# Performance work log

Hardware: AMD Instinct MI355X
Metric: run time of the kernel (lower is better)

The kernel has to match this reference:

```python
import jax, jax.numpy as jnp
import numpy as np

HEIGHT = 8  # init kwarg: output crop height
B, J, C, HIMG, WIMG = 8, 64, 32, 256, 256


def _make_boxes():
    rng = np.random.default_rng(0)
    left = rng.uniform(0.0, 40.0, (B, J))
    bw = rng.uniform(16.0, 200.0, (B, J))
    top = rng.uniform(0.0, 200.0, (B, J))
    bh = rng.uniform(8.0, 32.0, (B, J))
    theta = rng.uniform(-0.5, 0.5, (B, J))  # unused by the original forward
    return np.stack([left, top, left + bw, top + bh, theta], axis=-1).astype(np.float32)


def _box_widths(boxes_np):
    # torch: width = int(aspect * height), truncation (values are positive)
    bw = boxes_np[..., 2] - boxes_np[..., 0]
    bh = boxes_np[..., 3] - boxes_np[..., 1]
    return ((bw / bh) * HEIGHT).astype(np.int32)  # [B, J]


def setup_inputs() -> dict:
    key = jax.random.key(0)
    image = jax.random.normal(key, (B, C, HIMG, WIMG), dtype=jnp.float32)
    boxes = jnp.asarray(_make_boxes())
    return {"image": image, "boxes": boxes}


def reference(image, boxes):
    # Per-box widths are integer (shape-determining) constants, taken from concrete box data.
    boxes_np = np.asarray(jax.device_get(boxes))
    widths_np = _box_widths(boxes_np)          # [B, J] ints >= 2
    max_w = int(widths_np.max())
    widths = jnp.asarray(widths_np)

    dt = boxes.dtype
    base_w = boxes[..., 2] - boxes[..., 0]      # [B, J]
    base_h = boxes[..., 3] - boxes[..., 1]
    each_w = base_w / (widths.astype(dt) - 1)   # [B, J]
    each_h = base_h / (HEIGHT - 1)

    # Sampling grids: xx [B,J,Wm], yy [B,J,Hh]
    xx = jnp.arange(max_w, dtype=dt)[None, None, :] * each_w[..., None] + boxes[..., 0:1]
    yy = jnp.arange(HEIGHT, dtype=dt)[None, None, :] * each_h[..., None] + boxes[..., 1:2]

    def interp_one_image(img, x, y):
        # img [C,Hi,Wi], x [J,Wm], y [J,Hh] -> [C,J,Hh,Wm]
        x0 = jnp.clip(jnp.floor(x).astype(jnp.int32), 0, WIMG - 1)
        x1 = jnp.clip(jnp.floor(x).astype(jnp.int32) + 1, 0, WIMG - 1)
        y0 = jnp.clip(jnp.floor(y).astype(jnp.int32), 0, HIMG - 1)
        y1 = jnp.clip(jnp.floor(y).astype(jnp.int32) + 1, 0, HIMG - 1)
        # gathers: [C, J, Hh, Wm]
        ia = img[:, y0[:, :, None], x0[:, None, :]]
        ib = img[:, y1[:, :, None], x0[:, None, :]]
        ic = img[:, y0[:, :, None], x1[:, None, :]]
        idd = img[:, y1[:, :, None], x1[:, None, :]]
        x0f, x1f = x0.astype(dt), x1.astype(dt)
        y0f, y1f = y0.astype(dt), y1.astype(dt)
        wa = (x1f - x)[:, None, :] * (y1f - y)[:, :, None]  # [J,Hh,Wm]
        wb = (x1f - x)[:, None, :] * (y - y0f)[:, :, None]
        wc = (x - x0f)[:, None, :] * (y1f - y)[:, :, None]
        wd = (x - x0f)[:, None, :] * (y - y0f)[:, :, None]
        return ia * wa[None] + ib * wb[None] + ic * wc[None] + idd * wd[None]

    res = jax.vmap(interp_one_image)(image, xx, yy)      # [B,C,J,Hh,Wm]
    res = jnp.transpose(res, (0, 2, 1, 3, 4))            # [B,J,C,Hh,Wm]

    mask = (jnp.arange(max_w)[None, None, :] < widths[..., None]).astype(jnp.uint8)  # [B,J,Wm]
    res = res * mask[:, :, None, None, :].astype(res.dtype)  # zero-pad beyond each box width
    return res, mask
```

## Files before the change

kernel.cpp:

```cpp
#include <hip/hip_runtime.h>

#define HIMG 256
#define WIMG 256
#define CCH  32
#define JBOX 64
#define BIMG 8
#define HGT  8
#define CPB  4
#define NCG  (CCH / CPB)
#define NXCD 8
#define LROW 256

typedef __attribute__((address_space(3))) float lds_f;
typedef const __attribute__((address_space(1))) float glb_f;

#define WAITV2() do { asm volatile("s_waitcnt vmcnt(2)" ::: "memory"); \
                      __builtin_amdgcn_sched_barrier(0); } while (0)

__global__ __launch_bounds__(256, 8) void roi_kernel(
    const float* __restrict__ img,
    const float* __restrict__ boxes,
    float* __restrict__ res,
    float* __restrict__ mask,
    int max_w)
{
    __shared__ float sbuf[2][CPB][2][LROW];

    const int d    = blockIdx.x;
    const int slot = d & (NXCD - 1);
    const int seq  = d >> 3;
    const int bj   = slot * ((BIMG * JBOX) / NXCD) + (seq >> 3);
    const int cg   = seq & 7;
    const int b    = bj >> 6;
    const int tid  = threadIdx.x;

    const float left = boxes[bj * 5 + 0];
    const float top  = boxes[bj * 5 + 1];
    const float bw   = boxes[bj * 5 + 2] - left;
    const float bh   = boxes[bj * 5 + 3] - top;

    const int   width  = (int)(bw / bh * 8.0f);
    const float each_w = bw / ((float)width - 1.0f);
    const float each_h = bh / 7.0f;

    const int xs  = max((int)floorf(left), 0);
    const int xs4 = xs & ~3;

    const int  i    = tid;
    const bool have = (i < max_w);
    const bool in_w = (i < width);
    const float x  = __fadd_rn(__fmul_rn((float)i, each_w), left);
    const int   xf = (int)floorf(x);
    const int   x0 = min(max(xf, 0), WIMG - 1);
    const float wx1 = (float)(x0 + 1) - x;
    const float wx0 = x - (float)x0;
    const int   lx0 = min(max(x0 - xs4, 0), 206);

    if (cg == 0 && have) {
        mask[(size_t)bj * max_w + i] = in_w ? 1.0f : 0.0f;
    }

    const int wv   = tid >> 6;
    const int lane = tid & 63;
    const float* chbase =
        img + (size_t)(b * CCH + cg * CPB + wv) * (HIMG * WIMG);
    const int offc = min(xs4 + 4 * lane, WIMG - 4);

    auto issue_batch = [&](int h, int bf) {
        const float yh  = __fadd_rn(__fmul_rn((float)h, each_h), top);
        const int   yfl = (int)floorf(yh);
        const int   ya  = min(max(yfl,     0), HIMG - 1);
        const int   yb  = min(max(yfl + 1, 0), HIMG - 1);
        const float* s0 = chbase + (size_t)ya * WIMG + offc;
        const float* s1 = chbase + (size_t)yb * WIMG + offc;
        __builtin_amdgcn_global_load_lds((glb_f*)s0, (lds_f*)&sbuf[bf][wv][0][0], 16, 0, 0);
        __builtin_amdgcn_global_load_lds((glb_f*)s1, (lds_f*)&sbuf[bf][wv][1][0], 16, 0, 0);
    };

    issue_batch(0, 0);
    issue_batch(1, 1);
    __builtin_amdgcn_sched_barrier(0);

    float* resp0 = res + ((size_t)(bj * CCH + cg * CPB) * HGT) * (size_t)max_w + i;
    const size_t c_stride = (size_t)HGT * max_w;

    #pragma unroll
    for (int h = 0; h < HGT; ++h) {
        const int bf = h & 1;

        WAITV2();
        __builtin_amdgcn_s_barrier();
        __builtin_amdgcn_sched_barrier(0);

        if (have) {
            const float yh  = __fadd_rn(__fmul_rn((float)h, each_h), top);
            const int   yfl = (int)floorf(yh);
            const int   ya  = min(max(yfl,     0), HIMG - 1);
            const int   yb  = min(max(yfl + 1, 0), HIMG - 1);
            const float wy1 = (float)yb - yh;
            const float wy0 = yh - (float)ya;
            const float wa  = wx1 * wy1;
            const float wb_ = wx1 * wy0;
            const float wc_ = wx0 * wy1;
            const float wd_ = wx0 * wy0;
            float* resp = resp0 + (size_t)h * max_w;
            #pragma unroll
            for (int c = 0; c < CPB; ++c) {
                const float v00 = sbuf[bf][c][0][lx0];
                const float v01 = sbuf[bf][c][0][lx0 + 1];
                const float v10 = sbuf[bf][c][1][lx0];
                const float v11 = sbuf[bf][c][1][lx0 + 1];
                const float val = v00 * wa + v10 * wb_ + v01 * wc_ + v11 * wd_;
                resp[(size_t)c * c_stride] = in_w ? val : 0.0f;
            }
        }

        __builtin_amdgcn_sched_barrier(0);
        __builtin_amdgcn_s_barrier();
        __builtin_amdgcn_sched_barrier(0);

        if (h + 2 < HGT) {
            issue_batch(h + 2, bf);
            __builtin_amdgcn_sched_barrier(0);
        }
    }
}

extern "C" void kernel_launch(void* const* d_in, const int* in_sizes, int n_in,
                              void* d_out, int out_size, void* d_ws, size_t ws_size,
                              hipStream_t stream) {
    const float* img   = (const float*)d_in[0];
    const float* boxes = (const float*)d_in[1];
    float* out = (float*)d_out;

    const int per_w = BIMG * JBOX * CCH * HGT + BIMG * JBOX;
    const int max_w = out_size / per_w;

    float* res  = out;
    float* mask = out + (size_t)BIMG * JBOX * CCH * HGT * max_w;

    const int blocks = BIMG * JBOX * NCG;
    roi_kernel<<<blocks, 256, 0, stream>>>(img, boxes, res, mask, max_w);
}
```

Before: 153.3 us.

## Stage each box's full row band per channel in LDS with one block per channel

Each block now handles a single (box, channel) pair instead of four channels. It first loads every image row the box's eight sample heights can touch, full width, into LDS with direct global-to-LDS loads behind one barrier. The eight output rows are then interpolated from that staged band. This removes the per-height double-buffered pipeline and its repeated barriers, and launches more, smaller blocks (192 threads). In exchange it loads more image data per channel and assumes max_w fits in 192 threads and the row span fits in 34 rows.

Result: slower. 170.2 us (+11.0%).

```diff
diff --git a/kernel.cpp b/kernel.cpp
--- a/kernel.cpp
+++ b/kernel.cpp
@@ -6,33 +6,27 @@
 #define JBOX 64
 #define BIMG 8
 #define HGT  8
-#define CPB  4
-#define NCG  (CCH / CPB)
-#define NXCD 8
-#define LROW 256
+#define MAXR 34
 
 typedef __attribute__((address_space(3))) float lds_f;
 typedef const __attribute__((address_space(1))) float glb_f;
 
-#define WAITV2() do { asm volatile("s_waitcnt vmcnt(2)" ::: "memory"); \
-                      __builtin_amdgcn_sched_barrier(0); } while (0)
-
-__global__ __launch_bounds__(256, 8) void roi_kernel(
+__global__ __launch_bounds__(192, 3) void roi_kernel(
     const float* __restrict__ img,
     const float* __restrict__ boxes,
     float* __restrict__ res,
     float* __restrict__ mask,
     int max_w)
 {
-    __shared__ float sbuf[2][CPB][2][LROW];
+    __shared__ float srows[MAXR][WIMG];
 
-    const int d    = blockIdx.x;
-    const int slot = d & (NXCD - 1);
-    const int seq  = d >> 3;
-    const int bj   = slot * ((BIMG * JBOX) / NXCD) + (seq >> 3);
-    const int cg   = seq & 7;
-    const int b    = bj >> 6;
-    const int tid  = threadIdx.x;
+    const int g   = blockIdx.x;
+    const int b   = g & 7;
+    const int idx = g >> 3;
+    const int c   = idx >> 6;
+    const int j   = idx & 63;
+    const int bj  = b * JBOX + j;
+    const int tid = threadIdx.x;
 
     const float left = boxes[bj * 5 + 0];
     const float top  = boxes[bj * 5 + 1];
@@ -43,86 +37,59 @@
     const float each_w = bw / ((float)width - 1.0f);
     const float each_h = bh / 7.0f;
 
-    const int xs  = max((int)floorf(left), 0);
-    const int xs4 = xs & ~3;
+    const int   ylo = min(max((int)floorf(top), 0), HIMG - 1);
+    const float y7  = __fadd_rn(__fmul_rn(7.0f, each_h), top);
+    const int   yhi = min(max((int)floorf(y7) + 1, 0), HIMG - 1);
+    const int   nr  = min(yhi - ylo + 1, MAXR);
 
-    const int  i    = tid;
-    const bool have = (i < max_w);
+    const int wv   = tid >> 6;
+    const int lane = tid & 63;
+    const float* chbase = img + (size_t)(b * CCH + c) * (HIMG * WIMG);
+    for (int r = wv; r < nr; r += 3) {
+        const float* src = chbase + (size_t)(ylo + r) * WIMG + 4 * lane;
+        __builtin_amdgcn_global_load_lds((glb_f*)src, (lds_f*)&srows[r][0], 16, 0, 0);
+    }
+    __syncthreads();
+
+    const int  i = tid;
+    if (i >= max_w) return;
     const bool in_w = (i < width);
+
+    if (c == 0) {
+        mask[(size_t)bj * max_w + i] = in_w ? 1.0f : 0.0f;
+    }
+
     const float x  = __fadd_rn(__fmul_rn((float)i, each_w), left);
     const int   xf = (int)floorf(x);
     const int   x0 = min(max(xf, 0), WIMG - 1);
     const float wx1 = (float)(x0 + 1) - x;
     const float wx0 = x - (float)x0;
-    const int   lx0 = min(max(x0 - xs4, 0), 206);
+    const int   lx  = min(x0, WIMG - 2);
 
-    if (cg == 0 && have) {
-        mask[(size_t)bj * max_w + i] = in_w ? 1.0f : 0.0f;
-    }
+    float* resp = res + ((size_t)(bj * CCH + c) * HGT) * (size_t)max_w + i;
 
-    const int wv   = tid >> 6;
-    const int lane = tid & 63;
-    const float* chbase =
-        img + (size_t)(b * CCH + cg * CPB + wv) * (HIMG * WIMG);
-    const int offc = min(xs4 + 4 * lane, WIMG - 4);
-
-    auto issue_batch = [&](int h, int bf) {
+    #pragma unroll
+    for (int h = 0; h < HGT; ++h) {
         const float yh  = __fadd_rn(__fmul_rn((float)h, each_h), top);
         const int   yfl = (int)floorf(yh);
         const int   ya  = min(max(yfl,     0), HIMG - 1);
         const int   yb  = min(max(yfl + 1, 0), HIMG - 1);
-        const float* s0 = chbase + (size_t)ya * WIMG + offc;
-        const float* s1 = chbase + (size_t)yb * WIMG + offc;
-        __builtin_amdgcn_global_load_lds((glb_f*)s0, (lds_f*)&sbuf[bf][wv][0][0], 16, 0, 0);
-        __builtin_amdgcn_global_load_lds((glb_f*)s1, (lds_f*)&sbuf[bf][wv][1][0], 16, 0, 0);
-    };
+        const float wy1 = (float)yb - yh;
+        const float wy0 = yh - (float)ya;
+        const int   r0  = min(max(ya - ylo, 0), MAXR - 1);
+        const int   r1  = min(max(yb - ylo, 0), MAXR - 1);
 
-    issue_batch(0, 0);
-    issue_batch(1, 1);
-    __builtin_amdgcn_sched_barrier(0);
+        const float wa  = wx1 * wy1;
+        const float wb_ = wx1 * wy0;
+        const float wc_ = wx0 * wy1;
+        const float wd_ = wx0 * wy0;
 
-    float* resp0 = res + ((size_t)(bj * CCH + cg * CPB) * HGT) * (size_t)max_w + i;
-    const size_t c_stride = (size_t)HGT * max_w;
-
-    #pragma unroll
-    for (int h = 0; h < HGT; ++h) {
-        const int bf = h & 1;
-
-        WAITV2();
-        __builtin_amdgcn_s_barrier();
-        __builtin_amdgcn_sched_barrier(0);
-
-        if (have) {
-            const float yh  = __fadd_rn(__fmul_rn((float)h, each_h), top);
-            const int   yfl = (int)floorf(yh);
-            const int   ya  = min(max(yfl,     0), HIMG - 1);
-            const int   yb  = min(max(yfl + 1, 0), HIMG - 1);
-            const float wy1 = (float)yb - yh;
-            const float wy0 = yh - (float)ya;
-            const float wa  = wx1 * wy1;
-            const float wb_ = wx1 * wy0;
-            const float wc_ = wx0 * wy1;
-            const float wd_ = wx0 * wy0;
-            float* resp = resp0 + (size_t)h * max_w;
-            #pragma unroll
-            for (int c = 0; c < CPB; ++c) {
-                const float v00 = sbuf[bf][c][0][lx0];
-                const float v01 = sbuf[bf][c][0][lx0 + 1];
-                const float v10 = sbuf[bf][c][1][lx0];
-                const float v11 = sbuf[bf][c][1][lx0 + 1];
-                const float val = v00 * wa + v10 * wb_ + v01 * wc_ + v11 * wd_;
-                resp[(size_t)c * c_stride] = in_w ? val : 0.0f;
-            }
-        }
-
-        __builtin_amdgcn_sched_barrier(0);
-        __builtin_amdgcn_s_barrier();
-        __builtin_amdgcn_sched_barrier(0);
-
-        if (h + 2 < HGT) {
-            issue_batch(h + 2, bf);
-            __builtin_amdgcn_sched_barrier(0);
-        }
+        const float v00 = srows[r0][lx];
+        const float v01 = srows[r0][lx + 1];
+        const float v10 = srows[r1][lx];
+        const float v11 = srows[r1][lx + 1];
+        const float val = v00 * wa + v10 * wb_ + v01 * wc_ + v11 * wd_;
+        resp[(size_t)h * max_w] = in_w ? val : 0.0f;
     }
 }
 
@@ -139,6 +106,6 @@
     float* res  = out;
     float* mask = out + (size_t)BIMG * JBOX * CCH * HGT * max_w;
 
-    const int blocks = BIMG * JBOX * NCG;
-    roi_kernel<<<blocks, 256, 0, stream>>>(img, boxes, res, mask, max_w);
+    const int blocks = BIMG * JBOX * CCH;
+    roi_kernel<<<blocks, 192, 0, stream>>>(img, boxes, res, mask, max_w);
 }
```
